# Performance work log

Hardware: AMD Instinct MI355X
Metric: run time of the kernel (lower is better)

The kernel has to match this reference:

```python
import jax, jax.numpy as jnp
import numpy as np

B, T, H, A, V, L = 4096, 16, 768, 128, 16, 2

def setup_inputs() -> dict:
    key = jax.random.key(0)
    ks = jax.random.split(key, 8)
    s = 0.02
    return {
        "last_hidden": jax.random.normal(ks[0], (B, T, H), jnp.float32),
        "attention_mask": jnp.ones((B, T), jnp.int64),
        "variety_ids": jax.random.randint(ks[1], (B,), 0, V),
        "Wd": jax.random.normal(ks[2], (V, H, A), jnp.float32) * s,  # per-variety down-proj
        "bd": jnp.zeros((V, A), jnp.float32),
        "Wu": jax.random.normal(ks[3], (V, A, H), jnp.float32) * s,  # per-variety up-proj
        "bu": jnp.zeros((V, H), jnp.float32),
        "Wc": jax.random.normal(ks[4], (L, H), jnp.float32) * s,     # classifier
        "bc": jnp.zeros((L,), jnp.float32),
    }

def reference(last_hidden, attention_mask, variety_ids, Wd, bd, Wu, bu, Wc, bc):
    x = last_hidden[:, 0, :]                                   # (B,H) CLS token
    # Dense grouped adapter: run all V bottleneck adapters, then select per example.
    h = jax.nn.gelu(jnp.einsum('bh,vha->bva', x, Wd) + bd[None])   # (B,V,A)
    u = jnp.einsum('bva,vah->bvh', h, Wu) + bu[None]               # (B,V,H)
    sel = u[jnp.arange(x.shape[0]), variety_ids]                   # (B,H) routed output
    adapted = x + sel                                              # residual bottleneck adapter
    # dropout is identity at p=0.0 / eval
    return adapted @ Wc.T + bc                                     # (B,L) logits
```

## Files before the change

kernel.cpp:

```cpp
#include <hip/hip_runtime.h>
#include <hip/hip_bf16.h>

#define BB 4096
#define TT 16
#define HH 768
#define AA 128
#define VV 16
#define LL 2
#define NCHUNK 6
#define MT 16

typedef __attribute__((ext_vector_type(8))) short short8v;
typedef __attribute__((ext_vector_type(4))) float float4v;

#define WS_OFFS 0
#define WS_ROWS 64
#define WS_WUC  4160
#define WS_BUC  8256
#define WS_WDP  8448

__device__ __forceinline__ unsigned short f2bf(float f) {
    __hip_bfloat16 h = __float2bfloat16(f);
    return *reinterpret_cast<unsigned short*>(&h);
}

__device__ __forceinline__ float gelu_tanh(float z) {
    float y = 0.7978845608028654f * (z + 0.044715f * z * z * z);
    y = fminf(fmaxf(y, -15.f), 15.f);
    float e = __expf(2.f * y);
    float th = (e - 1.f) / (e + 1.f);
    return 0.5f * z * (1.f + th);
}

__global__ __launch_bounds__(256) void k_prep(
    const int*   __restrict__ variety_ids,
    const float* __restrict__ Wd,
    const float* __restrict__ Wu,
    const float* __restrict__ bu,
    const float* __restrict__ Wc,
    int* __restrict__ ws_i)
{
    __shared__ __align__(16) unsigned short Wds[128 * 136];
    __shared__ float sp0[256], sp1[256];
    __shared__ int hist[VV], hoff[VV + 1], hcur[VV];

    const int t = threadIdx.x;
    const int bid = blockIdx.x;
    unsigned short* wdp = (unsigned short*)(ws_i + WS_WDP);
    float* Wuc = (float*)(ws_i + WS_WUC);
    float* buc = (float*)(ws_i + WS_BUC);

    if (bid < 96) {
        const int v = bid / NCHUNK, kc = bid % NCHUNK;
        const float* wd = Wd + (size_t)v * HH * AA;
        const int ks0 = kc * 128;
        #pragma unroll
        for (int s = 0; s < 16; ++s) {
            int idx = t + s * 256;
            int hl  = idx >> 5;
            int a4  = idx & 31;
            float4 wv = *(const float4*)(wd + (size_t)(ks0 + hl) * AA + a4 * 4);
            Wds[(a4 * 4 + 0) * 136 + hl] = f2bf(wv.x);
            Wds[(a4 * 4 + 1) * 136 + hl] = f2bf(wv.y);
            Wds[(a4 * 4 + 2) * 136 + hl] = f2bf(wv.z);
            Wds[(a4 * 4 + 3) * 136 + hl] = f2bf(wv.w);
        }
        __syncthreads();
        unsigned short* dst = wdp + (size_t)(v * NCHUNK + kc) * AA * 128;
        #pragma unroll
        for (int s = 0; s < 8; ++s) {
            int G = t + s * 256;
            int a = G >> 4, g = G & 15;
            uint4 w = *(const uint4*)&Wds[a * 136 + g * 8];
            *(uint4*)&dst[a * 128 + g * 8] = w;
        }
    } else if (bid < 224) {
        const int v = (bid - 96) >> 3;
        const int g = (bid - 96) & 7;
        const int a_loc = t >> 4;
        const int q     = t & 15;
        const int a = g * 16 + a_loc;
        const float* wu = Wu + (size_t)v * AA * HH + (size_t)a * HH;
        float s0 = 0.f, s1 = 0.f;
        #pragma unroll 4
        for (int h = q * 48; h < q * 48 + 48; h += 4) {
            float4 w  = *(const float4*)&wu[h];
            float4 c0 = *(const float4*)&Wc[h];
            float4 c1 = *(const float4*)&Wc[HH + h];
            s0 += w.x * c0.x + w.y * c0.y + w.z * c0.z + w.w * c0.w;
            s1 += w.x * c1.x + w.y * c1.y + w.z * c1.z + w.w * c1.w;
        }
        sp0[a_loc * 16 + q] = s0;
        sp1[a_loc * 16 + q] = s1;
        __syncthreads();
        if (t < 16) {
            float r0 = 0.f, r1 = 0.f;
            #pragma unroll
            for (int i = 0; i < 16; ++i) { r0 += sp0[t * 16 + i]; r1 += sp1[t * 16 + i]; }
            int aa = g * 16 + t;
            Wuc[(v * AA + aa) * LL + 0] = r0;
            Wuc[(v * AA + aa) * LL + 1] = r1;
        }
    } else if (bid == 224) {
        const int pair = t >> 3, seg = t & 7;
        const int v = pair >> 1, l = pair & 1;
        float s = 0.f;
        const float* bv = bu + (size_t)v * HH;
        for (int h = seg * 96; h < seg * 96 + 96; ++h) s += bv[h] * Wc[l * HH + h];
        sp0[t] = s;
        __syncthreads();
        if (t < 32) {
            float r = 0.f;
            #pragma unroll
            for (int i = 0; i < 8; ++i) r += sp0[t * 8 + i];
            buc[t] = r;
        }
    } else {
        if (t < VV) hist[t] = 0;
        __syncthreads();
        for (int b = t; b < BB; b += 256) atomicAdd(&hist[variety_ids[b]], 1);
        __syncthreads();
        if (t == 0) {
            int s = 0;
            for (int i = 0; i < VV; ++i) { hoff[i] = s; s += hist[i]; }
            hoff[VV] = s;
            for (int i = 0; i <= VV; ++i) ws_i[WS_OFFS + i] = hoff[i];
        }
        __syncthreads();
        if (t < VV) hcur[t] = hoff[t];
        __syncthreads();
        for (int b = t; b < BB; b += 256) {
            int v = variety_ids[b];
            int p = atomicAdd(&hcur[v], 1);
            ws_i[WS_ROWS + p] = b;
        }
    }
}

__global__ __launch_bounds__(256) void k_main(
    const float* __restrict__ last_hidden,
    const int*   __restrict__ ws_i,
    const float* __restrict__ bd,
    const float* __restrict__ Wc,
    const float* __restrict__ bc,
    float* __restrict__ out)
{
    __shared__ __align__(16) unsigned short Xs[MT * 136];
    __shared__ __align__(16) unsigned short Wds[128 * 136];
    __shared__ __align__(16) unsigned short WcB[16 * 136];
    __shared__ int srows[MT];
    __shared__ float xc[MT * LL];

    const int* offs = ws_i + WS_OFFS;
    const int* rows = ws_i + WS_ROWS;
    const float* Wuc = (const float*)(ws_i + WS_WUC);
    const float* buc = (const float*)(ws_i + WS_BUC);
    const unsigned short* wdp = (const unsigned short*)(ws_i + WS_WDP);
    const int t = threadIdx.x;

    const int rt = blockIdx.x;
    int v = -1, tloc = 0, cnt = 0, obase = 0, acc_t = 0;
    for (int vv = 0; vv < VV; ++vv) {
        int c  = offs[vv + 1] - offs[vv];
        int nt = (c + MT - 1) / MT;
        if (rt < acc_t + nt) {
            v = vv; tloc = rt - acc_t;
            cnt = c - tloc * MT; if (cnt > MT) cnt = MT;
            obase = offs[vv];
            break;
        }
        acc_t += nt;
    }
    if (v < 0) return;

    if (t < MT) {
        int rr = t < cnt ? t : cnt - 1;
        srows[t] = rows[obase + tloc * MT + rr];
    }

    const int lane = t & 63;
    const int wv_  = t >> 6;
    const int ac0  = wv_ * 32;
    const int m = lane & 15, quad = lane >> 4;

    float4v acc[2];
    float4v accx;
    acc[0] = (float4v){0.f, 0.f, 0.f, 0.f};
    acc[1] = (float4v){0.f, 0.f, 0.f, 0.f};
    accx   = (float4v){0.f, 0.f, 0.f, 0.f};

    for (int kc = 0; kc < NCHUNK; ++kc) {
        const int ks0 = kc * 128;
        __syncthreads();
        #pragma unroll
        for (int s = 0; s < 2; ++s) {
            int idx = t + s * 256;
            int r   = idx >> 5;
            int k4  = idx & 31;
            const float* xr = last_hidden + (size_t)srows[r] * TT * HH + ks0 + k4 * 4;
            float4 xv = *(const float4*)xr;
            unsigned int p0 = (unsigned)f2bf(xv.x) | ((unsigned)f2bf(xv.y) << 16);
            unsigned int p1 = (unsigned)f2bf(xv.z) | ((unsigned)f2bf(xv.w) << 16);
            *(uint2*)&Xs[r * 136 + k4 * 4] = make_uint2(p0, p1);
        }
        {
            const unsigned short* wb = wdp + (size_t)(v * NCHUNK + kc) * AA * 128;
            #pragma unroll
            for (int s = 0; s < 8; ++s) {
                int G = t + s * 256;
                int a = G >> 4, g = G & 15;
                uint4 w = *(const uint4*)&wb[a * 128 + g * 8];
                *(uint4*)&Wds[a * 136 + g * 8] = w;
            }
        }
        {
            int c = t >> 4, g = t & 15;
            uint4 w = make_uint4(0u, 0u, 0u, 0u);
            if (c < LL) {
                const float* wcr = Wc + (size_t)c * HH + ks0 + g * 8;
                float4 w0 = *(const float4*)wcr;
                float4 w1 = *(const float4*)(wcr + 4);
                w.x = (unsigned)f2bf(w0.x) | ((unsigned)f2bf(w0.y) << 16);
                w.y = (unsigned)f2bf(w0.z) | ((unsigned)f2bf(w0.w) << 16);
                w.z = (unsigned)f2bf(w1.x) | ((unsigned)f2bf(w1.y) << 16);
                w.w = (unsigned)f2bf(w1.z) | ((unsigned)f2bf(w1.w) << 16);
            }
            *(uint4*)&WcB[c * 136 + g * 8] = w;
        }
        __syncthreads();

        #pragma unroll
        for (int k0 = 0; k0 < 128; k0 += 32) {
            short8v af = *(const short8v*)&Xs[m * 136 + k0 + quad * 8];
            short8v bf0 = *(const short8v*)&Wds[(ac0 + m) * 136 + k0 + quad * 8];
            short8v bf1 = *(const short8v*)&Wds[(ac0 + 16 + m) * 136 + k0 + quad * 8];
            acc[0] = __builtin_amdgcn_mfma_f32_16x16x32_bf16(af, bf0, acc[0], 0, 0, 0);
            acc[1] = __builtin_amdgcn_mfma_f32_16x16x32_bf16(af, bf1, acc[1], 0, 0, 0);
            if (wv_ == 0) {
                short8v cf = *(const short8v*)&WcB[m * 136 + k0 + quad * 8];
                accx = __builtin_amdgcn_mfma_f32_16x16x32_bf16(af, cf, accx, 0, 0, 0);
            }
        }
    }

    __syncthreads();
    float* p_part = (float*)Wds;

    {
        float bdv[2], w0v[2], w1v[2];
        #pragma unroll
        for (int j = 0; j < 2; ++j) {
            int a = ac0 + j * 16 + m;
            bdv[j] = bd[v * AA + a];
            w0v[j] = Wuc[(v * AA + a) * LL + 0];
            w1v[j] = Wuc[(v * AA + a) * LL + 1];
        }
        #pragma unroll
        for (int reg = 0; reg < 4; ++reg) {
            int row = quad * 4 + reg;
            float p0 = 0.f, p1 = 0.f;
            #pragma unroll
            for (int j = 0; j < 2; ++j) {
                float h = gelu_tanh(acc[j][reg] + bdv[j]);
                p0 += h * w0v[j];
                p1 += h * w1v[j];
            }
            p_part[(row * LL + 0) * 64 + wv_ * 16 + m] = p0;
            p_part[(row * LL + 1) * 64 + wv_ * 16 + m] = p1;
        }
        if (wv_ == 0 && m < LL) {
            #pragma unroll
            for (int reg = 0; reg < 4; ++reg) {
                int row = quad * 4 + reg;
                xc[row * LL + m] = accx[reg];
            }
        }
    }
    __syncthreads();

    if (t < MT * LL) {
        int row = t >> 1, l = t & 1;
        if (row < cnt) {
            float s = 0.f;
            #pragma unroll
            for (int k = 0; k < 64; ++k) s += p_part[(row * LL + l) * 64 + k];
            int gr = srows[row];
            out[(size_t)gr * LL + l] = s + xc[row * LL + l] + buc[v * LL + l] + bc[l];
        }
    }
}

extern "C" void kernel_launch(void* const* d_in, const int* in_sizes, int n_in,
                              void* d_out, int out_size, void* d_ws, size_t ws_size,
                              hipStream_t stream) {
    const float* last_hidden = (const float*)d_in[0];
    const int*   variety_ids = (const int*)d_in[2];
    const float* Wd = (const float*)d_in[3];
    const float* bd = (const float*)d_in[4];
    const float* Wu = (const float*)d_in[5];
    const float* bu = (const float*)d_in[6];
    const float* Wc = (const float*)d_in[7];
    const float* bc = (const float*)d_in[8];
    float* out = (float*)d_out;

    int* ws_i = (int*)d_ws;

    k_prep<<<226, 256, 0, stream>>>(variety_ids, Wd, Wu, bu, Wc, ws_i);
    k_main<<<271, 256, 0, stream>>>(last_hidden, ws_i, bd, Wc, bc, out);
}
```

Baseline: 271.3 us.

## Fuse prep and main kernels into one launch with per-block routing and weight prep

Merges the preprocessing kernel into the main kernel. Each block now builds the variety histogram with a packed wave-reduction, finds its own rows with a prefix scan, and computes the Wu·Wc and bu·Wc folds for its variety into shared memory. Wd is read and transposed to bf16 directly inside the chunk loop instead of from a pre-packed workspace copy. This removes one launch, the workspace round trip and the serial dependency between kernels. The cost is redundant work: every block rereads variety_ids and its variety's Wu, and uses slower transposing LDS stores for Wd.

```diff
diff --git a/kernel.cpp b/kernel.cpp
--- a/kernel.cpp
+++ b/kernel.cpp
@@ -13,12 +13,6 @@
 typedef __attribute__((ext_vector_type(8))) short short8v;
 typedef __attribute__((ext_vector_type(4))) float float4v;
 
-#define WS_OFFS 0
-#define WS_ROWS 64
-#define WS_WUC  4160
-#define WS_BUC  8256
-#define WS_WDP  8448
-
 __device__ __forceinline__ unsigned short f2bf(float f) {
     __hip_bfloat16 h = __float2bfloat16(f);
     return *reinterpret_cast<unsigned short*>(&h);
@@ -32,115 +26,13 @@
     return 0.5f * z * (1.f + th);
 }
 
-__global__ __launch_bounds__(256) void k_prep(
+__global__ __launch_bounds__(256) void k_fused(
+    const float* __restrict__ last_hidden,
     const int*   __restrict__ variety_ids,
     const float* __restrict__ Wd,
+    const float* __restrict__ bd,
     const float* __restrict__ Wu,
     const float* __restrict__ bu,
-    const float* __restrict__ Wc,
-    int* __restrict__ ws_i)
-{
-    __shared__ __align__(16) unsigned short Wds[128 * 136];
-    __shared__ float sp0[256], sp1[256];
-    __shared__ int hist[VV], hoff[VV + 1], hcur[VV];
-
-    const int t = threadIdx.x;
-    const int bid = blockIdx.x;
-    unsigned short* wdp = (unsigned short*)(ws_i + WS_WDP);
-    float* Wuc = (float*)(ws_i + WS_WUC);
-    float* buc = (float*)(ws_i + WS_BUC);
-
-    if (bid < 96) {
-        const int v = bid / NCHUNK, kc = bid % NCHUNK;
-        const float* wd = Wd + (size_t)v * HH * AA;
-        const int ks0 = kc * 128;
-        #pragma unroll
-        for (int s = 0; s < 16; ++s) {
-            int idx = t + s * 256;
-            int hl  = idx >> 5;
-            int a4  = idx & 31;
-            float4 wv = *(const float4*)(wd + (size_t)(ks0 + hl) * AA + a4 * 4);
-            Wds[(a4 * 4 + 0) * 136 + hl] = f2bf(wv.x);
-            Wds[(a4 * 4 + 1) * 136 + hl] = f2bf(wv.y);
-            Wds[(a4 * 4 + 2) * 136 + hl] = f2bf(wv.z);
-            Wds[(a4 * 4 + 3) * 136 + hl] = f2bf(wv.w);
-        }
-        __syncthreads();
-        unsigned short* dst = wdp + (size_t)(v * NCHUNK + kc) * AA * 128;
-        #pragma unroll
-        for (int s = 0; s < 8; ++s) {
-            int G = t + s * 256;
-            int a = G >> 4, g = G & 15;
-            uint4 w = *(const uint4*)&Wds[a * 136 + g * 8];
-            *(uint4*)&dst[a * 128 + g * 8] = w;
-        }
-    } else if (bid < 224) {
-        const int v = (bid - 96) >> 3;
-        const int g = (bid - 96) & 7;
-        const int a_loc = t >> 4;
-        const int q     = t & 15;
-        const int a = g * 16 + a_loc;
-        const float* wu = Wu + (size_t)v * AA * HH + (size_t)a * HH;
-        float s0 = 0.f, s1 = 0.f;
-        #pragma unroll 4
-        for (int h = q * 48; h < q * 48 + 48; h += 4) {
-            float4 w  = *(const float4*)&wu[h];
-            float4 c0 = *(const float4*)&Wc[h];
-            float4 c1 = *(const float4*)&Wc[HH + h];
-            s0 += w.x * c0.x + w.y * c0.y + w.z * c0.z + w.w * c0.w;
-            s1 += w.x * c1.x + w.y * c1.y + w.z * c1.z + w.w * c1.w;
-        }
-        sp0[a_loc * 16 + q] = s0;
-        sp1[a_loc * 16 + q] = s1;
-        __syncthreads();
-        if (t < 16) {
-            float r0 = 0.f, r1 = 0.f;
-            #pragma unroll
-            for (int i = 0; i < 16; ++i) { r0 += sp0[t * 16 + i]; r1 += sp1[t * 16 + i]; }
-            int aa = g * 16 + t;
-            Wuc[(v * AA + aa) * LL + 0] = r0;
-            Wuc[(v * AA + aa) * LL + 1] = r1;
-        }
-    } else if (bid == 224) {
-        const int pair = t >> 3, seg = t & 7;
-        const int v = pair >> 1, l = pair & 1;
-        float s = 0.f;
-        const float* bv = bu + (size_t)v * HH;
-        for (int h = seg * 96; h < seg * 96 + 96; ++h) s += bv[h] * Wc[l * HH + h];
-        sp0[t] = s;
-        __syncthreads();
-        if (t < 32) {
-            float r = 0.f;
-            #pragma unroll
-            for (int i = 0; i < 8; ++i) r += sp0[t * 8 + i];
-            buc[t] = r;
-        }
-    } else {
-        if (t < VV) hist[t] = 0;
-        __syncthreads();
-        for (int b = t; b < BB; b += 256) atomicAdd(&hist[variety_ids[b]], 1);
-        __syncthreads();
-        if (t == 0) {
-            int s = 0;
-            for (int i = 0; i < VV; ++i) { hoff[i] = s; s += hist[i]; }
-            hoff[VV] = s;
-            for (int i = 0; i <= VV; ++i) ws_i[WS_OFFS + i] = hoff[i];
-        }
-        __syncthreads();
-        if (t < VV) hcur[t] = hoff[t];
-        __syncthreads();
-        for (int b = t; b < BB; b += 256) {
-            int v = variety_ids[b];
-            int p = atomicAdd(&hcur[v], 1);
-            ws_i[WS_ROWS + p] = b;
-        }
-    }
-}
-
-__global__ __launch_bounds__(256) void k_main(
-    const float* __restrict__ last_hidden,
-    const int*   __restrict__ ws_i,
-    const float* __restrict__ bd,
     const float* __restrict__ Wc,
     const float* __restrict__ bc,
     float* __restrict__ out)
@@ -148,39 +40,144 @@
     __shared__ __align__(16) unsigned short Xs[MT * 136];
     __shared__ __align__(16) unsigned short Wds[128 * 136];
     __shared__ __align__(16) unsigned short WcB[16 * 136];
-    __shared__ int srows[MT];
+    __shared__ float Wuc_s[AA * LL];
+    __shared__ float buc_s[LL];
+    __shared__ int   hist[VV];
+    __shared__ int   srows[MT];
     __shared__ float xc[MT * LL];
-
-    const int* offs = ws_i + WS_OFFS;
-    const int* rows = ws_i + WS_ROWS;
-    const float* Wuc = (const float*)(ws_i + WS_WUC);
-    const float* buc = (const float*)(ws_i + WS_BUC);
-    const unsigned short* wdp = (const unsigned short*)(ws_i + WS_WDP);
-    const int t = threadIdx.x;
-
-    const int rt = blockIdx.x;
-    int v = -1, tloc = 0, cnt = 0, obase = 0, acc_t = 0;
-    for (int vv = 0; vv < VV; ++vv) {
-        int c  = offs[vv + 1] - offs[vv];
-        int nt = (c + MT - 1) / MT;
-        if (rt < acc_t + nt) {
-            v = vv; tloc = rt - acc_t;
-            cnt = c - tloc * MT; if (cnt > MT) cnt = MT;
-            obase = offs[vv];
-            break;
-        }
-        acc_t += nt;
+    __shared__ int   scanw[4];
+
+    const int t    = threadIdx.x;
+    const int lane = t & 63;
+    const int wid  = t >> 6;
+    const int rt   = blockIdx.x;
+
+    int ids[16];
+    {
+        const int4* vp = reinterpret_cast<const int4*>(variety_ids) + t * 4;
+        int4 A0 = vp[0], A1 = vp[1], A2 = vp[2], A3 = vp[3];
+        ids[0]=A0.x; ids[1]=A0.y; ids[2]=A0.z; ids[3]=A0.w;
+        ids[4]=A1.x; ids[5]=A1.y; ids[6]=A1.z; ids[7]=A1.w;
+        ids[8]=A2.x; ids[9]=A2.y; ids[10]=A2.z; ids[11]=A2.w;
+        ids[12]=A3.x; ids[13]=A3.y; ids[14]=A3.z; ids[15]=A3.w;
+    }
+    if (t < VV) hist[t] = 0;
+    __syncthreads();
+    {
+        unsigned long long p0 = 0, p1 = 0, p2 = 0, p3 = 0;
+        #pragma unroll
+        for (int i = 0; i < 16; ++i) {
+            int vv = ids[i];
+            unsigned long long inc = 1ull << ((vv & 3) * 16);
+            int w = vv >> 2;
+            p0 += (w == 0) ? inc : 0ull;
+            p1 += (w == 1) ? inc : 0ull;
+            p2 += (w == 2) ? inc : 0ull;
+            p3 += (w == 3) ? inc : 0ull;
+        }
+        #pragma unroll
+        for (int d = 1; d < 64; d <<= 1) {
+            p0 += __shfl_xor(p0, d);
+            p1 += __shfl_xor(p1, d);
+            p2 += __shfl_xor(p2, d);
+            p3 += __shfl_xor(p3, d);
+        }
+        if (lane < VV) {
+            int w = lane >> 2;
+            unsigned long long pw = (w == 0) ? p0 : (w == 1) ? p1 : (w == 2) ? p2 : p3;
+            int c = (int)((pw >> ((lane & 3) * 16)) & 0xffffull);
+            if (c) atomicAdd(&hist[lane], c);
+        }
+    }
+    __syncthreads();
+
+    int v = -1, tloc = 0, cnt = 0;
+    {
+        int acc_t = 0;
+        for (int vv = 0; vv < VV; ++vv) {
+            int c  = hist[vv];
+            int nt = (c + MT - 1) >> 4;
+            if (v < 0 && rt < acc_t + nt) {
+                v = vv; tloc = rt - acc_t;
+                cnt = c - tloc * MT; if (cnt > MT) cnt = MT;
+            }
+            acc_t += nt;
+        }
     }
     if (v < 0) return;
 
-    if (t < MT) {
-        int rr = t < cnt ? t : cnt - 1;
-        srows[t] = rows[obase + tloc * MT + rr];
-    }
-
-    const int lane = t & 63;
-    const int wv_  = t >> 6;
-    const int ac0  = wv_ * 32;
+    {
+        int m_t = 0;
+        #pragma unroll
+        for (int i = 0; i < 16; ++i) m_t += (ids[i] == v) ? 1 : 0;
+        int isc = m_t;
+        #pragma unroll
+        for (int d = 1; d < 64; d <<= 1) {
+            int y = __shfl_up(isc, d);
+            if (lane >= d) isc += y;
+        }
+        if (lane == 63) scanw[wid] = isc;
+        __syncthreads();
+        int base = 0;
+        #pragma unroll
+        for (int w = 0; w < 4; ++w) if (w < wid) base += scanw[w];
+        int r = base + isc - m_t - tloc * MT;
+        #pragma unroll
+        for (int i = 0; i < 16; ++i) {
+            if (ids[i] == v) {
+                if (r >= 0 && r < MT) srows[r] = t * 16 + i;
+                ++r;
+            }
+        }
+    }
+    __syncthreads();
+    if (t == 0 && cnt < MT) {
+        int last = srows[cnt - 1];
+        for (int i = cnt; i < MT; ++i) srows[i] = last;
+    }
+
+    {
+        const int a    = t >> 1;
+        const int half = t & 1;
+        const float* wu  = Wu + ((size_t)v * AA + a) * HH + half * 384;
+        const float* wcb = Wc + half * 384;
+        float s0 = 0.f, s1 = 0.f;
+        #pragma unroll 8
+        for (int h = 0; h < 384; h += 4) {
+            float4 w  = *(const float4*)(wu  + h);
+            float4 c0 = *(const float4*)(wcb + h);
+            float4 c1 = *(const float4*)(wcb + HH + h);
+            s0 += w.x * c0.x + w.y * c0.y + w.z * c0.z + w.w * c0.w;
+            s1 += w.x * c1.x + w.y * c1.y + w.z * c1.z + w.w * c1.w;
+        }
+        s0 += __shfl_xor(s0, 1);
+        s1 += __shfl_xor(s1, 1);
+        if (half == 0) { Wuc_s[a * LL + 0] = s0; Wuc_s[a * LL + 1] = s1; }
+    }
+
+    {
+        float* redbuf = (float*)Wds;
+        if (t < 128) {
+            const float* bv = bu + (size_t)v * HH + t * 6;
+            const float* c0 = Wc + t * 6;
+            const float* c1 = Wc + HH + t * 6;
+            float s0 = 0.f, s1 = 0.f;
+            #pragma unroll
+            for (int j = 0; j < 6; ++j) { s0 += bv[j] * c0[j]; s1 += bv[j] * c1[j]; }
+            redbuf[t] = s0; redbuf[128 + t] = s1;
+        }
+        __syncthreads();
+        if (wid == 0) {
+            float s0 = redbuf[lane] + redbuf[lane + 64];
+            float s1 = redbuf[128 + lane] + redbuf[192 + lane];
+            #pragma unroll
+            for (int d = 32; d; d >>= 1) { s0 += __shfl_xor(s0, d); s1 += __shfl_xor(s1, d); }
+            if (lane == 0) { buc_s[0] = s0; buc_s[1] = s1; }
+        }
+    }
+
+    const int wv_ = wid;
+    const int ac0 = wv_ * 32;
     const int m = lane & 15, quad = lane >> 4;
 
     float4v acc[2];
@@ -188,6 +185,8 @@
     acc[0] = (float4v){0.f, 0.f, 0.f, 0.f};
     acc[1] = (float4v){0.f, 0.f, 0.f, 0.f};
     accx   = (float4v){0.f, 0.f, 0.f, 0.f};
+
+    const float* wdv = Wd + (size_t)v * HH * AA;
 
     for (int kc = 0; kc < NCHUNK; ++kc) {
         const int ks0 = kc * 128;
@@ -199,19 +198,20 @@
             int k4  = idx & 31;
             const float* xr = last_hidden + (size_t)srows[r] * TT * HH + ks0 + k4 * 4;
             float4 xv = *(const float4*)xr;
-            unsigned int p0 = (unsigned)f2bf(xv.x) | ((unsigned)f2bf(xv.y) << 16);
-            unsigned int p1 = (unsigned)f2bf(xv.z) | ((unsigned)f2bf(xv.w) << 16);
-            *(uint2*)&Xs[r * 136 + k4 * 4] = make_uint2(p0, p1);
-        }
-        {
-            const unsigned short* wb = wdp + (size_t)(v * NCHUNK + kc) * AA * 128;
-            #pragma unroll
-            for (int s = 0; s < 8; ++s) {
-                int G = t + s * 256;
-                int a = G >> 4, g = G & 15;
-                uint4 w = *(const uint4*)&wb[a * 128 + g * 8];
-                *(uint4*)&Wds[a * 136 + g * 8] = w;
-            }
+            unsigned int q0 = (unsigned)f2bf(xv.x) | ((unsigned)f2bf(xv.y) << 16);
+            unsigned int q1 = (unsigned)f2bf(xv.z) | ((unsigned)f2bf(xv.w) << 16);
+            *(uint2*)&Xs[r * 136 + k4 * 4] = make_uint2(q0, q1);
+        }
+        #pragma unroll
+        for (int s = 0; s < 16; ++s) {
+            int idx = t + s * 256;
+            int hl  = idx >> 5;
+            int a4  = idx & 31;
+            float4 wv = *(const float4*)(wdv + (size_t)(ks0 + hl) * AA + a4 * 4);
+            Wds[(a4 * 4 + 0) * 136 + hl] = f2bf(wv.x);
+            Wds[(a4 * 4 + 1) * 136 + hl] = f2bf(wv.y);
+            Wds[(a4 * 4 + 2) * 136 + hl] = f2bf(wv.z);
+            Wds[(a4 * 4 + 3) * 136 + hl] = f2bf(wv.w);
         }
         {
             int c = t >> 4, g = t & 15;
@@ -231,7 +231,7 @@
 
         #pragma unroll
         for (int k0 = 0; k0 < 128; k0 += 32) {
-            short8v af = *(const short8v*)&Xs[m * 136 + k0 + quad * 8];
+            short8v af  = *(const short8v*)&Xs[m * 136 + k0 + quad * 8];
             short8v bf0 = *(const short8v*)&Wds[(ac0 + m) * 136 + k0 + quad * 8];
             short8v bf1 = *(const short8v*)&Wds[(ac0 + 16 + m) * 136 + k0 + quad * 8];
             acc[0] = __builtin_amdgcn_mfma_f32_16x16x32_bf16(af, bf0, acc[0], 0, 0, 0);
@@ -252,8 +252,8 @@
         for (int j = 0; j < 2; ++j) {
             int a = ac0 + j * 16 + m;
             bdv[j] = bd[v * AA + a];
-            w0v[j] = Wuc[(v * AA + a) * LL + 0];
-            w1v[j] = Wuc[(v * AA + a) * LL + 1];
+            w0v[j] = Wuc_s[a * LL + 0];
+            w1v[j] = Wuc_s[a * LL + 1];
         }
         #pragma unroll
         for (int reg = 0; reg < 4; ++reg) {
@@ -285,7 +285,7 @@
             #pragma unroll
             for (int k = 0; k < 64; ++k) s += p_part[(row * LL + l) * 64 + k];
             int gr = srows[row];
-            out[(size_t)gr * LL + l] = s + xc[row * LL + l] + buc[v * LL + l] + bc[l];
+            out[(size_t)gr * LL + l] = s + xc[row * LL + l] + buc_s[l] + bc[l];
         }
     }
 }
@@ -303,8 +303,5 @@
     const float* bc = (const float*)d_in[8];
     float* out = (float*)d_out;
 
-    int* ws_i = (int*)d_ws;
-
-    k_prep<<<226, 256, 0, stream>>>(variety_ids, Wd, Wu, bu, Wc, ws_i);
-    k_main<<<271, 256, 0, stream>>>(last_hidden, ws_i, bd, Wc, bc, out);
+    k_fused<<<271, 256, 0, stream>>>(last_hidden, variety_ids, Wd, bd, Wu, bu, Wc, bc, out);
 }
```

Measured after the change: 326.1 us. +20.2%, slower.

## Load Wd fragments directly into registers and double-buffer X with prefetch

Applied to the files above, without the earlier changes.

The Wd tile is now read from global memory straight into per-lane MFMA fragment registers rather than being staged through shared memory. The next chunk's X and Wd values are prefetched into registers while the current chunk computes. X uses a double-buffered shared tile, so only one barrier per chunk is needed. Wc is also loaded directly by wave 0. This cuts LDS traffic and barriers and overlaps global loads with MFMA work, at the cost of higher register pressure and less coalesced global reads of the fragments.

```diff
diff --git a/kernel.cpp b/kernel.cpp
--- a/kernel.cpp
+++ b/kernel.cpp
@@ -145,9 +145,8 @@
     const float* __restrict__ bc,
     float* __restrict__ out)
 {
-    __shared__ __align__(16) unsigned short Xs[MT * 136];
-    __shared__ __align__(16) unsigned short Wds[128 * 136];
-    __shared__ __align__(16) unsigned short WcB[16 * 136];
+    __shared__ __align__(16) unsigned short Xs[2][MT * 136];
+    __shared__ __align__(16) float p_part[MT * LL * 64];
     __shared__ int srows[MT];
     __shared__ float xc[MT * LL];
 
@@ -177,11 +176,20 @@
         int rr = t < cnt ? t : cnt - 1;
         srows[t] = rows[obase + tloc * MT + rr];
     }
+    __syncthreads();
 
     const int lane = t & 63;
     const int wv_  = t >> 6;
     const int ac0  = wv_ * 32;
     const int m = lane & 15, quad = lane >> 4;
+    const int r0 = t >> 5, k4 = t & 31;
+
+    const float* xb0 = last_hidden + (size_t)srows[r0]     * TT * HH + k4 * 4;
+    const float* xb1 = last_hidden + (size_t)srows[r0 + 8] * TT * HH + k4 * 4;
+    const unsigned short* wdv = wdp + (size_t)v * NCHUNK * AA * 128;
+    const unsigned short* bp0 = wdv + (size_t)(ac0 + m)      * 128 + quad * 8;
+    const unsigned short* bp1 = wdv + (size_t)(ac0 + 16 + m) * 128 + quad * 8;
+    const float* cfp = Wc + (size_t)m * HH + quad * 8;
 
     float4v acc[2];
     float4v accx;
@@ -189,62 +197,70 @@
     acc[1] = (float4v){0.f, 0.f, 0.f, 0.f};
     accx   = (float4v){0.f, 0.f, 0.f, 0.f};
 
+    float4 xA = *(const float4*)xb0;
+    float4 xB = *(const float4*)xb1;
+    short8v Bn[8];
+    #pragma unroll
+    for (int i = 0; i < 4; ++i) {
+        Bn[i]     = *(const short8v*)(bp0 + i * 32);
+        Bn[4 + i] = *(const short8v*)(bp1 + i * 32);
+    }
+
+    #pragma unroll
     for (int kc = 0; kc < NCHUNK; ++kc) {
-        const int ks0 = kc * 128;
-        __syncthreads();
-        #pragma unroll
-        for (int s = 0; s < 2; ++s) {
-            int idx = t + s * 256;
-            int r   = idx >> 5;
-            int k4  = idx & 31;
-            const float* xr = last_hidden + (size_t)srows[r] * TT * HH + ks0 + k4 * 4;
-            float4 xv = *(const float4*)xr;
-            unsigned int p0 = (unsigned)f2bf(xv.x) | ((unsigned)f2bf(xv.y) << 16);
-            unsigned int p1 = (unsigned)f2bf(xv.z) | ((unsigned)f2bf(xv.w) << 16);
-            *(uint2*)&Xs[r * 136 + k4 * 4] = make_uint2(p0, p1);
-        }
+        float4 xAc = xA, xBc = xB;
+        short8v Bc[8];
+        #pragma unroll
+        for (int i = 0; i < 8; ++i) Bc[i] = Bn[i];
+
+        if (kc + 1 < NCHUNK) {
+            xA = *(const float4*)(xb0 + (kc + 1) * 128);
+            xB = *(const float4*)(xb1 + (kc + 1) * 128);
+            #pragma unroll
+            for (int i = 0; i < 4; ++i) {
+                Bn[i]     = *(const short8v*)(bp0 + (size_t)(kc + 1) * AA * 128 + i * 32);
+                Bn[4 + i] = *(const short8v*)(bp1 + (size_t)(kc + 1) * AA * 128 + i * 32);
+            }
+        }
+
+        unsigned short* xs = (unsigned short*)Xs[kc & 1];
         {
-            const unsigned short* wb = wdp + (size_t)(v * NCHUNK + kc) * AA * 128;
-            #pragma unroll
-            for (int s = 0; s < 8; ++s) {
-                int G = t + s * 256;
-                int a = G >> 4, g = G & 15;
-                uint4 w = *(const uint4*)&wb[a * 128 + g * 8];
-                *(uint4*)&Wds[a * 136 + g * 8] = w;
-            }
-        }
-        {
-            int c = t >> 4, g = t & 15;
-            uint4 w = make_uint4(0u, 0u, 0u, 0u);
-            if (c < LL) {
-                const float* wcr = Wc + (size_t)c * HH + ks0 + g * 8;
-                float4 w0 = *(const float4*)wcr;
-                float4 w1 = *(const float4*)(wcr + 4);
-                w.x = (unsigned)f2bf(w0.x) | ((unsigned)f2bf(w0.y) << 16);
-                w.y = (unsigned)f2bf(w0.z) | ((unsigned)f2bf(w0.w) << 16);
-                w.z = (unsigned)f2bf(w1.x) | ((unsigned)f2bf(w1.y) << 16);
-                w.w = (unsigned)f2bf(w1.z) | ((unsigned)f2bf(w1.w) << 16);
-            }
-            *(uint4*)&WcB[c * 136 + g * 8] = w;
-        }
-        __syncthreads();
-
-        #pragma unroll
-        for (int k0 = 0; k0 < 128; k0 += 32) {
-            short8v af = *(const short8v*)&Xs[m * 136 + k0 + quad * 8];
-            short8v bf0 = *(const short8v*)&Wds[(ac0 + m) * 136 + k0 + quad * 8];
-            short8v bf1 = *(const short8v*)&Wds[(ac0 + 16 + m) * 136 + k0 + quad * 8];
-            acc[0] = __builtin_amdgcn_mfma_f32_16x16x32_bf16(af, bf0, acc[0], 0, 0, 0);
-            acc[1] = __builtin_amdgcn_mfma_f32_16x16x32_bf16(af, bf1, acc[1], 0, 0, 0);
+            unsigned int q0 = (unsigned)f2bf(xAc.x) | ((unsigned)f2bf(xAc.y) << 16);
+            unsigned int q1 = (unsigned)f2bf(xAc.z) | ((unsigned)f2bf(xAc.w) << 16);
+            *(uint2*)&xs[r0 * 136 + k4 * 4] = make_uint2(q0, q1);
+            q0 = (unsigned)f2bf(xBc.x) | ((unsigned)f2bf(xBc.y) << 16);
+            q1 = (unsigned)f2bf(xBc.z) | ((unsigned)f2bf(xBc.w) << 16);
+            *(uint2*)&xs[(r0 + 8) * 136 + k4 * 4] = make_uint2(q0, q1);
+        }
+        __syncthreads();
+
+        float4 cfa[8];
+        if (wv_ == 0 && m < LL) {
+            #pragma unroll
+            for (int i = 0; i < 4; ++i) {
+                cfa[2 * i]     = *(const float4*)(cfp + kc * 128 + i * 32);
+                cfa[2 * i + 1] = *(const float4*)(cfp + kc * 128 + i * 32 + 4);
+            }
+        }
+
+        #pragma unroll
+        for (int i = 0; i < 4; ++i) {
+            short8v af = *(const short8v*)&xs[m * 136 + i * 32 + quad * 8];
+            acc[0] = __builtin_amdgcn_mfma_f32_16x16x32_bf16(af, Bc[i],     acc[0], 0, 0, 0);
+            acc[1] = __builtin_amdgcn_mfma_f32_16x16x32_bf16(af, Bc[4 + i], acc[1], 0, 0, 0);
             if (wv_ == 0) {
-                short8v cf = *(const short8v*)&WcB[m * 136 + k0 + quad * 8];
+                short8v cf = (short8v){0, 0, 0, 0, 0, 0, 0, 0};
+                if (m < LL) {
+                    float4 c0 = cfa[2 * i], c1 = cfa[2 * i + 1];
+                    cf[0] = (short)f2bf(c0.x); cf[1] = (short)f2bf(c0.y);
+                    cf[2] = (short)f2bf(c0.z); cf[3] = (short)f2bf(c0.w);
+                    cf[4] = (short)f2bf(c1.x); cf[5] = (short)f2bf(c1.y);
+                    cf[6] = (short)f2bf(c1.z); cf[7] = (short)f2bf(c1.w);
+                }
                 accx = __builtin_amdgcn_mfma_f32_16x16x32_bf16(af, cf, accx, 0, 0, 0);
             }
         }
     }
-
-    __syncthreads();
-    float* p_part = (float*)Wds;
 
     {
         float bdv[2], w0v[2], w1v[2];
```

Measured after the change: 269.1 us (median of 2 runs). Within noise of the previous version (-0.8%).
